# Optimization experiments

Hardware: AMD Instinct MI355X
Metric: run time of the kernel (lower is better)

## Reference

```python
import jax, jax.numpy as jnp
import numpy as np

B, S, H = 1, 1024, 2880
NQ, NKV, D = 64, 8, 64          # query heads, kv heads, head_dim
G = NQ // NKV                    # GQA group size
W = 128                          # sliding window
SCALE = D ** -0.5
NEG = -1e30


def rotate_half(x):
    x1, x2 = jnp.split(x, 2, axis=-1)
    return jnp.concatenate((-x2, x1), axis=-1)


def setup_inputs() -> dict:
    key = jax.random.key(0)
    ks = jax.random.split(key, 8)
    hidden_states = jax.random.normal(ks[0], (B, S, H), jnp.float32)
    # rotary tables, half head_dim (module concats (cos,cos) to full dim)
    pos = jnp.arange(S, dtype=jnp.float32)[:, None]
    inv = 1.0 / (10000.0 ** (jnp.arange(0, D, 2, dtype=jnp.float32) / D))
    ang = pos * inv[None, :]                      # (S, D/2)
    cos = jnp.cos(ang)[None].astype(jnp.float32)  # (1, S, D/2)
    sin = jnp.sin(ang)[None].astype(jnp.float32)
    w_qkv = jax.random.normal(ks[1], (H, (NQ + 2 * NKV) * D), jnp.float32) * 0.02
    b_qkv = jax.random.normal(ks[2], ((NQ + 2 * NKV) * D,), jnp.float32) * 0.02
    w_o = jax.random.normal(ks[3], (NQ * D, H), jnp.float32) * 0.02
    b_o = jax.random.normal(ks[4], (H,), jnp.float32) * 0.02
    sinks = jax.random.normal(ks[5], (NQ,), jnp.float32)
    k_cache = jnp.zeros((B, S, NKV, D), jnp.float32)
    v_cache = jnp.zeros((B, S, NKV, D), jnp.float32)
    return {"hidden_states": hidden_states, "cos": cos, "sin": sin,
            "w_qkv": w_qkv, "b_qkv": b_qkv, "w_o": w_o, "b_o": b_o,
            "sinks": sinks, "k_cache": k_cache, "v_cache": v_cache, "kv_len": 0}


def reference(hidden_states, cos, sin, w_qkv, b_qkv, w_o, b_o, sinks,
              k_cache, v_cache, kv_len):
    # fused QKV projection + split
    qkv = hidden_states @ w_qkv + b_qkv                      # (B, S, (NQ+2*NKV)*D)
    q, k, v = jnp.split(qkv, [NQ * D, NQ * D + NKV * D], axis=-1)
    q = q.reshape(B, S, NQ, D)
    k = k.reshape(B, S, NKV, D)
    v = v.reshape(B, S, NKV, D)
    # RoPE (BSND layout, half-dim tables duplicated to full dim)
    cosf = jnp.concatenate((cos, cos), axis=-1)[:, :, None, :]
    sinf = jnp.concatenate((sin, sin), axis=-1)[:, :, None, :]
    q = q * cosf + rotate_half(q) * sinf
    k = k * cosf + rotate_half(k) * sinf
    # KV-cache scatter update at position kv_len along seq dim
    k_cache = jax.lax.dynamic_update_slice(k_cache, k, (0, kv_len, 0, 0))
    v_cache = jax.lax.dynamic_update_slice(v_cache, v, (0, kv_len, 0, 0))
    T = kv_len + S
    keys = k_cache[:, :T]                                    # (B, T, NKV, D)
    vals = v_cache[:, :T]
    # GQA: group query heads by kv head
    qg = q.reshape(B, S, NKV, G, D)
    scores = jnp.einsum('bqhgd,bkhd->bhgqk', qg, keys) * SCALE  # (B,NKV,G,S,T)
    # causal + sliding-window mask
    i = jnp.arange(S)[:, None] + kv_len
    j = jnp.arange(T)[None, :]
    allowed = (j <= i) & (i - j < W)
    scores = jnp.where(allowed, scores, NEG)
    # softmax with per-head learnable sink logit (sink gets no value)
    sk = sinks.reshape(NKV, G)[None, :, :, None]             # (1,NKV,G,1)
    m = jnp.maximum(jnp.max(scores, axis=-1), sk)            # (B,NKV,G,S)
    p = jnp.exp(scores - m[..., None])
    denom = jnp.sum(p, axis=-1) + jnp.exp(sk - m)
    attn = jnp.einsum('bhgqk,bkhd->bqhgd', p / denom[..., None], vals)
    out = attn.reshape(B, S, NQ * D) @ w_o + b_o             # (B, S, H)
    return out
```

## Files before the change

kernel.cpp:

```cpp
#include <hip/hip_runtime.h>
#include <hip/hip_bf16.h>

#define NQH 64
#define NKVH 8
#define DH 64
#define SEQ 1024
#define HID 2880
#define QKV_N 5120
#define ATTN_N 4096
#define WIN 128
#define WO_NPAD 2944
#define SCALE_F 0.125f

typedef __attribute__((ext_vector_type(8))) __bf16 bf16x8;
typedef __attribute__((ext_vector_type(4))) float f32x4;

#define GLOAD_LDS16(g, l) \
    __builtin_amdgcn_global_load_lds((const __attribute__((address_space(1))) void*)(g), \
                                     (__attribute__((address_space(3))) void*)(l), 16, 0, 0)

__device__ __forceinline__ ushort f2bf(float x) {
    union { float f; unsigned int u; } c; c.f = x;
    unsigned int u = c.u;
    unsigned int r = (u + 0x7FFFu + ((u >> 16) & 1u)) >> 16;
    return (ushort)r;
}

__global__ __launch_bounds__(256) void convert_f32_bf16(
    const float* __restrict__ in, ushort* __restrict__ out, int n4)
{
    int idx = blockIdx.x * blockDim.x + threadIdx.x;
    int stride = gridDim.x * blockDim.x;
    for (int i = idx; i < n4; i += stride) {
        float4 v = reinterpret_cast<const float4*>(in)[i];
        ushort4 o;
        o.x = f2bf(v.x); o.y = f2bf(v.y); o.z = f2bf(v.z); o.w = f2bf(v.w);
        reinterpret_cast<ushort4*>(out)[i] = o;
    }
}

__global__ __launch_bounds__(256) void transpose_convert(
    const float* __restrict__ in, ushort* __restrict__ out, int K, int N)
{
    __shared__ ushort tile[64][80];
    const int bk = blockIdx.x * 64;
    const int bn = blockIdx.y * 64;
    const int tid = threadIdx.x;
    const bool inb = bn < N;

#pragma unroll
    for (int it = 0; it < 4; ++it) {
        int r = it * 16 + (tid >> 4);
        int c4 = (tid & 15) * 4;
        float4 v = make_float4(0.f, 0.f, 0.f, 0.f);
        if (inb) v = *(const float4*)&in[(size_t)(bk + r) * N + bn + c4];
        tile[c4 + 0][r] = f2bf(v.x);
        tile[c4 + 1][r] = f2bf(v.y);
        tile[c4 + 2][r] = f2bf(v.z);
        tile[c4 + 3][r] = f2bf(v.w);
    }
    __syncthreads();
#pragma unroll
    for (int it = 0; it < 2; ++it) {
        int nr = it * 32 + (tid >> 3);
        int c8 = (tid & 7) * 8;
        uint4 v = *(const uint4*)&tile[nr][c8];
        *(uint4*)&out[(size_t)(bn + nr) * K + bk + c8] = v;
    }
}

template<bool ROPE>
__global__ __launch_bounds__(256) void gemm128sq(
    const ushort* __restrict__ A, const ushort* __restrict__ BT,
    const float* __restrict__ bias, float* __restrict__ C,
    int K, int ldC, int Nreal,
    const float* __restrict__ cosp, const float* __restrict__ sinp)
{
    __shared__ ushort Al[2 * 8192];
    __shared__ ushort Bl[2 * 8192];
    const int t = threadIdx.x;
    const int lane = t & 63;
    const int w = t >> 6;
    const int wr = w >> 1, wc = w & 1;
    const int g4 = lane >> 4;
    const int r15 = lane & 15;

    const int flat = blockIdx.x + gridDim.x * blockIdx.y;
    const int per = (gridDim.x * gridDim.y) >> 3;
    const int virt = (flat & 7) * per + (flat >> 3);
    const int m0 = (virt & 7) * 128;
    const int n0 = (virt >> 3) * 128;

    const ushort* aSrc[4]; const ushort* bSrc[4]; int dOff[4];
#pragma unroll
    for (int i = 0; i < 4; ++i) {
        int lin = i * 256 + t;
        int row = lin >> 3;
        int ch = (lin & 7) ^ (row & 7);
        aSrc[i] = A  + (size_t)(m0 + row) * K + ch * 8;
        bSrc[i] = BT + (size_t)(n0 + row) * K + ch * 8;
        dOff[i] = lin * 8;
    }

#define STAGE_TILE(buf) do { \
        _Pragma("unroll") \
        for (int i = 0; i < 4; ++i) { \
            GLOAD_LDS16(aSrc[i], &Al[(buf) * 8192 + dOff[i]]); \
            GLOAD_LDS16(bSrc[i], &Bl[(buf) * 8192 + dOff[i]]); \
            aSrc[i] += 64; bSrc[i] += 64; \
        } \
    } while (0)

    int aoff[4][2], boff[4][2];
#pragma unroll
    for (int i = 0; i < 4; ++i)
#pragma unroll
        for (int ks = 0; ks < 2; ++ks) {
            int row = wr * 64 + i * 16 + r15;
            aoff[i][ks] = row * 64 + (((ks * 4 + g4) ^ (row & 7)) * 8);
            int col = wc * 64 + i * 16 + r15;
            boff[i][ks] = col * 64 + (((ks * 4 + g4) ^ (col & 7)) * 8);
        }

    f32x4 acc[4][4];
#pragma unroll
    for (int mi = 0; mi < 4; ++mi)
#pragma unroll
        for (int ni = 0; ni < 4; ++ni) acc[mi][ni] = (f32x4){0.f, 0.f, 0.f, 0.f};

#define COMPUTE_TILE(buf) do { \
        const ushort* Ab = &Al[(buf) * 8192]; \
        const ushort* Bb = &Bl[(buf) * 8192]; \
        _Pragma("unroll") \
        for (int ks = 0; ks < 2; ++ks) { \
            bf16x8 af0 = *(const bf16x8*)&Ab[aoff[0][ks]]; \
            bf16x8 af1 = *(const bf16x8*)&Ab[aoff[1][ks]]; \
            bf16x8 af2 = *(const bf16x8*)&Ab[aoff[2][ks]]; \
            bf16x8 af3 = *(const bf16x8*)&Ab[aoff[3][ks]]; \
            bf16x8 bf0 = *(const bf16x8*)&Bb[boff[0][ks]]; \
            bf16x8 bf1 = *(const bf16x8*)&Bb[boff[1][ks]]; \
            bf16x8 bf2 = *(const bf16x8*)&Bb[boff[2][ks]]; \
            bf16x8 bf3 = *(const bf16x8*)&Bb[boff[3][ks]]; \
            acc[0][0] = __builtin_amdgcn_mfma_f32_16x16x32_bf16(af0, bf0, acc[0][0], 0, 0, 0); \
            acc[0][1] = __builtin_amdgcn_mfma_f32_16x16x32_bf16(af0, bf1, acc[0][1], 0, 0, 0); \
            acc[0][2] = __builtin_amdgcn_mfma_f32_16x16x32_bf16(af0, bf2, acc[0][2], 0, 0, 0); \
            acc[0][3] = __builtin_amdgcn_mfma_f32_16x16x32_bf16(af0, bf3, acc[0][3], 0, 0, 0); \
            acc[1][0] = __builtin_amdgcn_mfma_f32_16x16x32_bf16(af1, bf0, acc[1][0], 0, 0, 0); \
            acc[1][1] = __builtin_amdgcn_mfma_f32_16x16x32_bf16(af1, bf1, acc[1][1], 0, 0, 0); \
            acc[1][2] = __builtin_amdgcn_mfma_f32_16x16x32_bf16(af1, bf2, acc[1][2], 0, 0, 0); \
            acc[1][3] = __builtin_amdgcn_mfma_f32_16x16x32_bf16(af1, bf3, acc[1][3], 0, 0, 0); \
            acc[2][0] = __builtin_amdgcn_mfma_f32_16x16x32_bf16(af2, bf0, acc[2][0], 0, 0, 0); \
            acc[2][1] = __builtin_amdgcn_mfma_f32_16x16x32_bf16(af2, bf1, acc[2][1], 0, 0, 0); \
            acc[2][2] = __builtin_amdgcn_mfma_f32_16x16x32_bf16(af2, bf2, acc[2][2], 0, 0, 0); \
            acc[2][3] = __builtin_amdgcn_mfma_f32_16x16x32_bf16(af2, bf3, acc[2][3], 0, 0, 0); \
            acc[3][0] = __builtin_amdgcn_mfma_f32_16x16x32_bf16(af3, bf0, acc[3][0], 0, 0, 0); \
            acc[3][1] = __builtin_amdgcn_mfma_f32_16x16x32_bf16(af3, bf1, acc[3][1], 0, 0, 0); \
            acc[3][2] = __builtin_amdgcn_mfma_f32_16x16x32_bf16(af3, bf2, acc[3][2], 0, 0, 0); \
            acc[3][3] = __builtin_amdgcn_mfma_f32_16x16x32_bf16(af3, bf3, acc[3][3], 0, 0, 0); \
        } \
    } while (0)

    const int NT = K >> 6;
    STAGE_TILE(0);
    __syncthreads();
    for (int kt = 0; kt < NT; kt += 2) {
        if (kt + 1 < NT) STAGE_TILE(1);
        COMPUTE_TILE(0);
        __syncthreads();
        if (kt + 1 < NT) {
            if (kt + 2 < NT) STAGE_TILE(0);
            COMPUTE_TILE(1);
            __syncthreads();
        }
    }
#undef STAGE_TILE
#undef COMPUTE_TILE

#pragma unroll
    for (int ni = 0; ni < 4; ++ni) {
        int col = n0 + wc * 64 + ni * 16 + r15;
        float bv = (col < Nreal) ? bias[col] : 0.f;
#pragma unroll
        for (int mi = 0; mi < 4; ++mi)
#pragma unroll
            for (int r = 0; r < 4; ++r) acc[mi][ni][r] += bv;
    }
    if (ROPE) {
        const int head = (n0 + wc * 64) >> 6;
        if (head < 72) {
#pragma unroll
            for (int mi = 0; mi < 4; ++mi)
#pragma unroll
                for (int r = 0; r < 4; ++r) {
                    int q = m0 + wr * 64 + mi * 16 + g4 * 4 + r;
#pragma unroll
                    for (int dp = 0; dp < 2; ++dp) {
                        int d = dp * 16 + r15;
                        float c = cosp[q * 32 + d];
                        float s = sinp[q * 32 + d];
                        float x1 = acc[mi][dp][r];
                        float x2 = acc[mi][dp + 2][r];
                        acc[mi][dp][r]     = x1 * c - x2 * s;
                        acc[mi][dp + 2][r] = x2 * c + x1 * s;
                    }
                }
        }
    }
#pragma unroll
    for (int ni = 0; ni < 4; ++ni) {
        int col = n0 + wc * 64 + ni * 16 + r15;
        if (col < Nreal) {
#pragma unroll
            for (int mi = 0; mi < 4; ++mi) {
                int row = m0 + wr * 64 + mi * 16 + g4 * 4;
#pragma unroll
                for (int r = 0; r < 4; ++r)
                    C[(size_t)(row + r) * ldC + col] = acc[mi][ni][r];
            }
        }
    }
}

__global__ __launch_bounds__(512) void attn_mfma_kernel(
    const float* __restrict__ qkv, const float* __restrict__ sinks,
    ushort* __restrict__ attn_out)
{
    __shared__ __align__(16) ushort Kl[160][72];
    __shared__ __align__(16) ushort Vt[64][168];
    __shared__ __align__(16) ushort Pl[8][32][40];
    const int t = threadIdx.x;
    const int w = t >> 6;
    const int l = t & 63;
    const int g4 = l >> 4;
    const int r15 = l & 15;
    const int q0 = blockIdx.x * 32;
    const int hk = blockIdx.y;
    const int kbase = q0 - 128;

#pragma unroll
    for (int i = 0; i < 5; ++i) {
        int idx = i * 512 + t;
        int row = idx >> 4;
        int c4 = (idx & 15) * 4;
        int j = kbase + row;
        float4 kv = make_float4(0.f, 0.f, 0.f, 0.f);
        float4 vv = make_float4(0.f, 0.f, 0.f, 0.f);
        if (j >= 0) {
            kv = *(const float4*)&qkv[(size_t)j * QKV_N + 4096 + hk * 64 + c4];
            vv = *(const float4*)&qkv[(size_t)j * QKV_N + 4608 + hk * 64 + c4];
        }
        ushort4 kp;
        kp.x = f2bf(kv.x); kp.y = f2bf(kv.y); kp.z = f2bf(kv.z); kp.w = f2bf(kv.w);
        *(ushort4*)&Kl[row][c4] = kp;
        Vt[c4 + 0][row] = f2bf(vv.x);
        Vt[c4 + 1][row] = f2bf(vv.y);
        Vt[c4 + 2][row] = f2bf(vv.z);
        Vt[c4 + 3][row] = f2bf(vv.w);
    }

    bf16x8 qf[2][2];
#pragma unroll
    for (int ct = 0; ct < 2; ++ct) {
        int R = w * 32 + ct * 16 + r15;
        int q = q0 + (R & 31);
        int hq = hk * 8 + (R >> 5);
        const float* qb = &qkv[(size_t)q * QKV_N + hq * 64];
#pragma unroll
        for (int s = 0; s < 2; ++s) {
            float4 a = *(const float4*)&qb[s * 32 + g4 * 8];
            float4 b = *(const float4*)&qb[s * 32 + g4 * 8 + 4];
            union { ushort u[8]; bf16x8 v; } pk;
            pk.u[0] = f2bf(a.x * SCALE_F); pk.u[1] = f2bf(a.y * SCALE_F);
            pk.u[2] = f2bf(a.z * SCALE_F); pk.u[3] = f2bf(a.w * SCALE_F);
            pk.u[4] = f2bf(b.x * SCALE_F); pk.u[5] = f2bf(b.y * SCALE_F);
            pk.u[6] = f2bf(b.z * SCALE_F); pk.u[7] = f2bf(b.w * SCALE_F);
            qf[ct][s] = pk.v;
        }
    }
    __syncthreads();

    f32x4 sc[10][2];
#pragma unroll
    for (int kt = 0; kt < 10; ++kt) {
        sc[kt][0] = (f32x4){0.f, 0.f, 0.f, 0.f};
        sc[kt][1] = (f32x4){0.f, 0.f, 0.f, 0.f};
    }
#pragma unroll
    for (int kt = 0; kt < 10; ++kt) {
#pragma unroll
        for (int s = 0; s < 2; ++s) {
            bf16x8 kf = *(const bf16x8*)&Kl[kt * 16 + r15][s * 32 + g4 * 8];
            sc[kt][0] = __builtin_amdgcn_mfma_f32_16x16x32_bf16(kf, qf[0][s], sc[kt][0], 0, 0, 0);
            sc[kt][1] = __builtin_amdgcn_mfma_f32_16x16x32_bf16(kf, qf[1][s], sc[kt][1], 0, 0, 0);
        }
    }

    const int minkey = 128 - q0;
#pragma unroll
    for (int ct = 0; ct < 2; ++ct) {
        int R = w * 32 + ct * 16 + r15;
        int ql = R & 31;
        float snk = sinks[hk * 8 + (R >> 5)];
#pragma unroll
        for (int kt = 0; kt < 10; ++kt)
#pragma unroll
            for (int r = 0; r < 4; ++r) {
                int key = kt * 16 + g4 * 4 + r;
                bool ok = (key > ql) && (key <= ql + 128) && (key >= minkey);
                if (!ok) sc[kt][ct][r] = -1e30f;
            }
        float m = snk;
#pragma unroll
        for (int kt = 0; kt < 10; ++kt)
#pragma unroll
            for (int r = 0; r < 4; ++r) m = fmaxf(m, sc[kt][ct][r]);
        m = fmaxf(m, __shfl_xor(m, 16));
        m = fmaxf(m, __shfl_xor(m, 32));
        float sum = 0.f;
#pragma unroll
        for (int kt = 0; kt < 10; ++kt)
#pragma unroll
            for (int r = 0; r < 4; ++r) {
                float p = __expf(sc[kt][ct][r] - m);
                sc[kt][ct][r] = p;
                sum += p;
            }
        sum += __shfl_xor(sum, 16);
        sum += __shfl_xor(sum, 32);
        sum += __expf(snk - m);
        float iv = 1.0f / sum;
#pragma unroll
        for (int kt = 0; kt < 10; ++kt)
#pragma unroll
            for (int r = 0; r < 4; ++r) sc[kt][ct][r] *= iv;
    }

    f32x4 pv[2][4];
#pragma unroll
    for (int mi = 0; mi < 2; ++mi)
#pragma unroll
        for (int ni = 0; ni < 4; ++ni) pv[mi][ni] = (f32x4){0.f, 0.f, 0.f, 0.f};

#pragma unroll
    for (int s = 0; s < 5; ++s) {
#pragma unroll
        for (int ct = 0; ct < 2; ++ct)
#pragma unroll
            for (int kh = 0; kh < 2; ++kh) {
                int kt = 2 * s + kh;
                ushort4 p4;
                p4.x = f2bf(sc[kt][ct][0]);
                p4.y = f2bf(sc[kt][ct][1]);
                p4.z = f2bf(sc[kt][ct][2]);
                p4.w = f2bf(sc[kt][ct][3]);
                *(ushort4*)&Pl[w][ct * 16 + r15][kh * 16 + g4 * 4] = p4;
            }
#pragma unroll
        for (int mi = 0; mi < 2; ++mi) {
            bf16x8 pf = *(const bf16x8*)&Pl[w][mi * 16 + r15][g4 * 8];
#pragma unroll
            for (int ni = 0; ni < 4; ++ni) {
                bf16x8 vf = *(const bf16x8*)&Vt[ni * 16 + r15][s * 32 + g4 * 8];
                pv[mi][ni] = __builtin_amdgcn_mfma_f32_16x16x32_bf16(pf, vf, pv[mi][ni], 0, 0, 0);
            }
        }
    }

#pragma unroll
    for (int mi = 0; mi < 2; ++mi)
#pragma unroll
        for (int r = 0; r < 4; ++r) {
            int R = w * 32 + mi * 16 + g4 * 4 + r;
            int q = q0 + (R & 31);
            int hq = hk * 8 + (R >> 5);
            ushort* ob = &attn_out[(size_t)q * ATTN_N + hq * 64 + r15];
#pragma unroll
            for (int ni = 0; ni < 4; ++ni)
                ob[ni * 16] = f2bf(pv[mi][ni][r]);
        }
}

extern "C" void kernel_launch(void* const* d_in, const int* in_sizes, int n_in,
                              void* d_out, int out_size, void* d_ws, size_t ws_size,
                              hipStream_t stream)
{
    const float* hidden = (const float*)d_in[0];
    const float* cosp   = (const float*)d_in[1];
    const float* sinp   = (const float*)d_in[2];
    const float* w_qkv  = (const float*)d_in[3];
    const float* b_qkv  = (const float*)d_in[4];
    const float* w_o    = (const float*)d_in[5];
    const float* b_o    = (const float*)d_in[6];
    const float* sinks  = (const float*)d_in[7];

    char* ws = (char*)d_ws;
    size_t off = 0;
    ushort* wqkvT = (ushort*)(ws + off); off += (size_t)QKV_N * HID * 2;
    ushort* woT   = (ushort*)(ws + off); off += (size_t)WO_NPAD * ATTN_N * 2;
    float*  qkv   = (float*)(ws + off);  off += (size_t)SEQ * QKV_N * 4;
    ushort* hidden_b = (ushort*)(ws + off);
    ushort* attn_b   = (ushort*)(ws + off); off += (size_t)SEQ * ATTN_N * 2;
    if (off > ws_size) return;

    transpose_convert<<<dim3(HID / 64, QKV_N / 64), 256, 0, stream>>>(w_qkv, wqkvT, HID, QKV_N);
    transpose_convert<<<dim3(ATTN_N / 64, WO_NPAD / 64), 256, 0, stream>>>(w_o, woT, ATTN_N, HID);
    convert_f32_bf16<<<2048, 256, 0, stream>>>(hidden, hidden_b, SEQ * HID / 4);

    gemm128sq<true><<<dim3(QKV_N / 128, SEQ / 128), 256, 0, stream>>>(
        hidden_b, wqkvT, b_qkv, qkv, HID, QKV_N, QKV_N, cosp, sinp);

    attn_mfma_kernel<<<dim3(SEQ / 32, NKVH), 512, 0, stream>>>(qkv, sinks, attn_b);

    gemm128sq<false><<<dim3(WO_NPAD / 128, SEQ / 128), 256, 0, stream>>>(
        attn_b, woT, b_o, (float*)d_out, ATTN_N, HID, HID, nullptr, nullptr);
}
```

Baseline: 162.8 us.

## Replace 128x128 four-wave GEMM with single-wave 64x64 tiles and waitcnt pipelining

The 256-thread 128x128 GEMM blocks become one-wave 64x64 blocks. Staging is double-buffered with direct global-to-LDS loads and ordered by explicit s_waitcnt vmcnt/lgkmcnt instead of __syncthreads. The aim is to drop block-wide barriers and to launch more, smaller blocks for better occupancy and overlap. In exchange each tile is reused less, so global and L2 traffic per FLOP roughly doubles.

Result: slower. 195.5 us (+20.1%).

```diff
diff --git a/kernel.cpp b/kernel.cpp
--- a/kernel.cpp
+++ b/kernel.cpp
@@ -70,107 +70,105 @@
 }
 
 template<bool ROPE>
-__global__ __launch_bounds__(256) void gemm128sq(
+__global__ __launch_bounds__(64) void gemm_wave(
     const ushort* __restrict__ A, const ushort* __restrict__ BT,
     const float* __restrict__ bias, float* __restrict__ C,
     int K, int ldC, int Nreal,
     const float* __restrict__ cosp, const float* __restrict__ sinp)
 {
-    __shared__ ushort Al[2 * 8192];
-    __shared__ ushort Bl[2 * 8192];
-    const int t = threadIdx.x;
-    const int lane = t & 63;
-    const int w = t >> 6;
-    const int wr = w >> 1, wc = w & 1;
+    __shared__ ushort Al[2 * 4096];
+    __shared__ ushort Bl[2 * 4096];
+    const int lane = threadIdx.x;
     const int g4 = lane >> 4;
     const int r15 = lane & 15;
 
     const int flat = blockIdx.x + gridDim.x * blockIdx.y;
     const int per = (gridDim.x * gridDim.y) >> 3;
     const int virt = (flat & 7) * per + (flat >> 3);
-    const int m0 = (virt & 7) * 128;
-    const int n0 = (virt >> 3) * 128;
-
-    const ushort* aSrc[4]; const ushort* bSrc[4]; int dOff[4];
-#pragma unroll
-    for (int i = 0; i < 4; ++i) {
-        int lin = i * 256 + t;
-        int row = lin >> 3;
-        int ch = (lin & 7) ^ (row & 7);
-        aSrc[i] = A  + (size_t)(m0 + row) * K + ch * 8;
-        bSrc[i] = BT + (size_t)(n0 + row) * K + ch * 8;
-        dOff[i] = lin * 8;
-    }
+    const int m0 = (virt & 15) * 64;
+    const int n0 = (virt >> 4) * 64;
+
+    const int srow = lane >> 3;
+    const int sch = (lane & 7) ^ srow;
+    const ushort* aBase = A  + (size_t)(m0 + srow) * K + sch * 8;
+    const ushort* bBase = BT + (size_t)(n0 + srow) * K + sch * 8;
+    const size_t rstep = (size_t)8 * K;
 
 #define STAGE_TILE(buf) do { \
+        const ushort* ap_ = aBase; const ushort* bp_ = bBase; \
         _Pragma("unroll") \
-        for (int i = 0; i < 4; ++i) { \
-            GLOAD_LDS16(aSrc[i], &Al[(buf) * 8192 + dOff[i]]); \
-            GLOAD_LDS16(bSrc[i], &Bl[(buf) * 8192 + dOff[i]]); \
-            aSrc[i] += 64; bSrc[i] += 64; \
+        for (int i_ = 0; i_ < 8; ++i_) { \
+            GLOAD_LDS16(ap_, &Al[(buf) * 4096 + i_ * 512]); \
+            GLOAD_LDS16(bp_, &Bl[(buf) * 4096 + i_ * 512]); \
+            ap_ += rstep; bp_ += rstep; \
+        } \
+        aBase += 64; bBase += 64; \
+    } while (0)
+
+    int aoff[4][2], boff[4][2];
+#pragma unroll
+    for (int i = 0; i < 4; ++i)
+#pragma unroll
+        for (int ks = 0; ks < 2; ++ks) {
+            int row = i * 16 + r15;
+            int slot = (ks * 4 + g4) ^ (row & 7);
+            aoff[i][ks] = row * 64 + slot * 8;
+            boff[i][ks] = row * 64 + slot * 8;
+        }
+
+    f32x4 acc[4][4];
+#pragma unroll
+    for (int mi = 0; mi < 4; ++mi)
+#pragma unroll
+        for (int ni = 0; ni < 4; ++ni) acc[mi][ni] = (f32x4){0.f, 0.f, 0.f, 0.f};
+
+#define COMPUTE_TILE(buf) do { \
+        const ushort* Ab = &Al[(buf) * 4096]; \
+        const ushort* Bb = &Bl[(buf) * 4096]; \
+        _Pragma("unroll") \
+        for (int ks = 0; ks < 2; ++ks) { \
+            bf16x8 a0 = *(const bf16x8*)&Ab[aoff[0][ks]]; \
+            bf16x8 a1 = *(const bf16x8*)&Ab[aoff[1][ks]]; \
+            bf16x8 a2 = *(const bf16x8*)&Ab[aoff[2][ks]]; \
+            bf16x8 a3 = *(const bf16x8*)&Ab[aoff[3][ks]]; \
+            bf16x8 b0 = *(const bf16x8*)&Bb[boff[0][ks]]; \
+            bf16x8 b1 = *(const bf16x8*)&Bb[boff[1][ks]]; \
+            bf16x8 b2 = *(const bf16x8*)&Bb[boff[2][ks]]; \
+            bf16x8 b3 = *(const bf16x8*)&Bb[boff[3][ks]]; \
+            acc[0][0] = __builtin_amdgcn_mfma_f32_16x16x32_bf16(a0, b0, acc[0][0], 0, 0, 0); \
+            acc[0][1] = __builtin_amdgcn_mfma_f32_16x16x32_bf16(a0, b1, acc[0][1], 0, 0, 0); \
+            acc[0][2] = __builtin_amdgcn_mfma_f32_16x16x32_bf16(a0, b2, acc[0][2], 0, 0, 0); \
+            acc[0][3] = __builtin_amdgcn_mfma_f32_16x16x32_bf16(a0, b3, acc[0][3], 0, 0, 0); \
+            acc[1][0] = __builtin_amdgcn_mfma_f32_16x16x32_bf16(a1, b0, acc[1][0], 0, 0, 0); \
+            acc[1][1] = __builtin_amdgcn_mfma_f32_16x16x32_bf16(a1, b1, acc[1][1], 0, 0, 0); \
+            acc[1][2] = __builtin_amdgcn_mfma_f32_16x16x32_bf16(a1, b2, acc[1][2], 0, 0, 0); \
+            acc[1][3] = __builtin_amdgcn_mfma_f32_16x16x32_bf16(a1, b3, acc[1][3], 0, 0, 0); \
+            acc[2][0] = __builtin_amdgcn_mfma_f32_16x16x32_bf16(a2, b0, acc[2][0], 0, 0, 0); \
+            acc[2][1] = __builtin_amdgcn_mfma_f32_16x16x32_bf16(a2, b1, acc[2][1], 0, 0, 0); \
+            acc[2][2] = __builtin_amdgcn_mfma_f32_16x16x32_bf16(a2, b2, acc[2][2], 0, 0, 0); \
+            acc[2][3] = __builtin_amdgcn_mfma_f32_16x16x32_bf16(a2, b3, acc[2][3], 0, 0, 0); \
+            acc[3][0] = __builtin_amdgcn_mfma_f32_16x16x32_bf16(a3, b0, acc[3][0], 0, 0, 0); \
+            acc[3][1] = __builtin_amdgcn_mfma_f32_16x16x32_bf16(a3, b1, acc[3][1], 0, 0, 0); \
+            acc[3][2] = __builtin_amdgcn_mfma_f32_16x16x32_bf16(a3, b2, acc[3][2], 0, 0, 0); \
+            acc[3][3] = __builtin_amdgcn_mfma_f32_16x16x32_bf16(a3, b3, acc[3][3], 0, 0, 0); \
         } \
     } while (0)
 
-    int aoff[4][2], boff[4][2];
-#pragma unroll
-    for (int i = 0; i < 4; ++i)
-#pragma unroll
-        for (int ks = 0; ks < 2; ++ks) {
-            int row = wr * 64 + i * 16 + r15;
-            aoff[i][ks] = row * 64 + (((ks * 4 + g4) ^ (row & 7)) * 8);
-            int col = wc * 64 + i * 16 + r15;
-            boff[i][ks] = col * 64 + (((ks * 4 + g4) ^ (col & 7)) * 8);
-        }
-
-    f32x4 acc[4][4];
-#pragma unroll
-    for (int mi = 0; mi < 4; ++mi)
-#pragma unroll
-        for (int ni = 0; ni < 4; ++ni) acc[mi][ni] = (f32x4){0.f, 0.f, 0.f, 0.f};
-
-#define COMPUTE_TILE(buf) do { \
-        const ushort* Ab = &Al[(buf) * 8192]; \
-        const ushort* Bb = &Bl[(buf) * 8192]; \
-        _Pragma("unroll") \
-        for (int ks = 0; ks < 2; ++ks) { \
-            bf16x8 af0 = *(const bf16x8*)&Ab[aoff[0][ks]]; \
-            bf16x8 af1 = *(const bf16x8*)&Ab[aoff[1][ks]]; \
-            bf16x8 af2 = *(const bf16x8*)&Ab[aoff[2][ks]]; \
-            bf16x8 af3 = *(const bf16x8*)&Ab[aoff[3][ks]]; \
-            bf16x8 bf0 = *(const bf16x8*)&Bb[boff[0][ks]]; \
-            bf16x8 bf1 = *(const bf16x8*)&Bb[boff[1][ks]]; \
-            bf16x8 bf2 = *(const bf16x8*)&Bb[boff[2][ks]]; \
-            bf16x8 bf3 = *(const bf16x8*)&Bb[boff[3][ks]]; \
-            acc[0][0] = __builtin_amdgcn_mfma_f32_16x16x32_bf16(af0, bf0, acc[0][0], 0, 0, 0); \
-            acc[0][1] = __builtin_amdgcn_mfma_f32_16x16x32_bf16(af0, bf1, acc[0][1], 0, 0, 0); \
-            acc[0][2] = __builtin_amdgcn_mfma_f32_16x16x32_bf16(af0, bf2, acc[0][2], 0, 0, 0); \
-            acc[0][3] = __builtin_amdgcn_mfma_f32_16x16x32_bf16(af0, bf3, acc[0][3], 0, 0, 0); \
-            acc[1][0] = __builtin_amdgcn_mfma_f32_16x16x32_bf16(af1, bf0, acc[1][0], 0, 0, 0); \
-            acc[1][1] = __builtin_amdgcn_mfma_f32_16x16x32_bf16(af1, bf1, acc[1][1], 0, 0, 0); \
-            acc[1][2] = __builtin_amdgcn_mfma_f32_16x16x32_bf16(af1, bf2, acc[1][2], 0, 0, 0); \
-            acc[1][3] = __builtin_amdgcn_mfma_f32_16x16x32_bf16(af1, bf3, acc[1][3], 0, 0, 0); \
-            acc[2][0] = __builtin_amdgcn_mfma_f32_16x16x32_bf16(af2, bf0, acc[2][0], 0, 0, 0); \
-            acc[2][1] = __builtin_amdgcn_mfma_f32_16x16x32_bf16(af2, bf1, acc[2][1], 0, 0, 0); \
-            acc[2][2] = __builtin_amdgcn_mfma_f32_16x16x32_bf16(af2, bf2, acc[2][2], 0, 0, 0); \
-            acc[2][3] = __builtin_amdgcn_mfma_f32_16x16x32_bf16(af2, bf3, acc[2][3], 0, 0, 0); \
-            acc[3][0] = __builtin_amdgcn_mfma_f32_16x16x32_bf16(af3, bf0, acc[3][0], 0, 0, 0); \
-            acc[3][1] = __builtin_amdgcn_mfma_f32_16x16x32_bf16(af3, bf1, acc[3][1], 0, 0, 0); \
-            acc[3][2] = __builtin_amdgcn_mfma_f32_16x16x32_bf16(af3, bf2, acc[3][2], 0, 0, 0); \
-            acc[3][3] = __builtin_amdgcn_mfma_f32_16x16x32_bf16(af3, bf3, acc[3][3], 0, 0, 0); \
-        } \
-    } while (0)
-
     const int NT = K >> 6;
     STAGE_TILE(0);
-    __syncthreads();
-    for (int kt = 0; kt < NT; kt += 2) {
-        if (kt + 1 < NT) STAGE_TILE(1);
-        COMPUTE_TILE(0);
-        __syncthreads();
+    STAGE_TILE(1);
+    for (int kt = 0; kt < NT; ++kt) {
         if (kt + 1 < NT) {
-            if (kt + 2 < NT) STAGE_TILE(0);
-            COMPUTE_TILE(1);
-            __syncthreads();
+            asm volatile("s_waitcnt vmcnt(16)" ::: "memory");
+        } else {
+            asm volatile("s_waitcnt vmcnt(0)" ::: "memory");
+        }
+        __builtin_amdgcn_sched_barrier(0);
+        COMPUTE_TILE(kt & 1);
+        if (kt + 2 < NT) {
+            asm volatile("s_waitcnt lgkmcnt(0)" ::: "memory");
+            __builtin_amdgcn_sched_barrier(0);
+            STAGE_TILE(kt & 1);
         }
     }
 #undef STAGE_TILE
@@ -178,7 +176,7 @@
 
 #pragma unroll
     for (int ni = 0; ni < 4; ++ni) {
-        int col = n0 + wc * 64 + ni * 16 + r15;
+        int col = n0 + ni * 16 + r15;
         float bv = (col < Nreal) ? bias[col] : 0.f;
 #pragma unroll
         for (int mi = 0; mi < 4; ++mi)
@@ -186,13 +184,13 @@
             for (int r = 0; r < 4; ++r) acc[mi][ni][r] += bv;
     }
     if (ROPE) {
-        const int head = (n0 + wc * 64) >> 6;
+        const int head = n0 >> 6;
         if (head < 72) {
 #pragma unroll
             for (int mi = 0; mi < 4; ++mi)
 #pragma unroll
                 for (int r = 0; r < 4; ++r) {
-                    int q = m0 + wr * 64 + mi * 16 + g4 * 4 + r;
+                    int q = m0 + mi * 16 + g4 * 4 + r;
 #pragma unroll
                     for (int dp = 0; dp < 2; ++dp) {
                         int d = dp * 16 + r15;
@@ -208,11 +206,11 @@
     }
 #pragma unroll
     for (int ni = 0; ni < 4; ++ni) {
-        int col = n0 + wc * 64 + ni * 16 + r15;
+        int col = n0 + ni * 16 + r15;
         if (col < Nreal) {
 #pragma unroll
             for (int mi = 0; mi < 4; ++mi) {
-                int row = m0 + wr * 64 + mi * 16 + g4 * 4;
+                int row = m0 + mi * 16 + g4 * 4;
 #pragma unroll
                 for (int r = 0; r < 4; ++r)
                     C[(size_t)(row + r) * ldC + col] = acc[mi][ni][r];
@@ -406,11 +404,11 @@
     transpose_convert<<<dim3(ATTN_N / 64, WO_NPAD / 64), 256, 0, stream>>>(w_o, woT, ATTN_N, HID);
     convert_f32_bf16<<<2048, 256, 0, stream>>>(hidden, hidden_b, SEQ * HID / 4);
 
-    gemm128sq<true><<<dim3(QKV_N / 128, SEQ / 128), 256, 0, stream>>>(
+    gemm_wave<true><<<dim3(QKV_N / 64, SEQ / 64), 64, 0, stream>>>(
         hidden_b, wqkvT, b_qkv, qkv, HID, QKV_N, QKV_N, cosp, sinp);
 
     attn_mfma_kernel<<<dim3(SEQ / 32, NKVH), 512, 0, stream>>>(qkv, sinks, attn_b);
 
-    gemm128sq<false><<<dim3(WO_NPAD / 128, SEQ / 128), 256, 0, stream>>>(
+    gemm_wave<false><<<dim3(WO_NPAD / 64, SEQ / 64), 64, 0, stream>>>(
         attn_b, woT, b_o, (float*)d_out, ATTN_N, HID, HID, nullptr, nullptr);
 }
```
